# Optimization experiments

Hardware: AMD Instinct MI355X
Metric: run time of the kernel (lower is better)

Reference implementation:

```python
import jax, jax.numpy as jnp
import numpy as np

B, T, C, H = 2, 2048, 1024, 16
N = C // H
TM_DIM, TD_DIM = 32, 64
EPS = 1e-5 * 8 ** 2  # GroupNorm eps from the module


def setup_inputs() -> dict:
    key = jax.random.key(0)
    ks = jax.random.split(key, 16)
    nrm = lambda k, shp, s: jax.random.normal(k, shp, dtype=jnp.float32) * s
    uni = lambda k, shp, a: jax.random.uniform(k, shp, jnp.float32, -a, a)
    ddd = (jnp.arange(C, dtype=jnp.float32) / C).reshape(1, 1, C)
    return {
        "x": nrm(ks[0], (B, T, C), 1.0),
        "time_maa_x": 1.0 - ddd ** 0.5,
        "time_maa_w": 1.0 - ddd ** 0.5,
        "time_maa_k": 1.0 - ddd ** 0.5,
        "time_maa_v": 1.0 - (ddd ** 0.5 + 0.15),
        "time_maa_r": 1.0 - ddd ** 0.25,
        "time_maa_g": 1.0 - ddd ** 0.25,
        "time_maa_w1": uni(ks[1], (C, 5 * TM_DIM), 1e-4),
        "time_maa_w2": uni(ks[2], (5, TM_DIM, C), 1e-4),
        "time_decay": jnp.linspace(-6.0, -1.0, C).astype(jnp.float32).reshape(1, 1, C),
        "time_decay_w1": uni(ks[3], (C, TD_DIM), 1e-4),
        "time_decay_w2": uni(ks[4], (TD_DIM, C), 1e-4),
        "time_faaaa": nrm(ks[5], (H, N), 0.1),
        "W_r": nrm(ks[6], (C, C), C ** -0.5),
        "W_k": nrm(ks[7], (C, C), C ** -0.5),
        "W_v": nrm(ks[8], (C, C), C ** -0.5),
        "W_g": nrm(ks[9], (C, C), C ** -0.5),
        "W_o": nrm(ks[10], (C, C), C ** -0.5),
        "ln_w": jnp.ones((C,), jnp.float32),
        "ln_b": jnp.zeros((C,), jnp.float32),
    }


def _forward(x, tmx, tmw, tmk, tmv, tmr, tmg, maa_w1, maa_w2, tdecay, td_w1,
             td_w2, u, Wr, Wk, Wv, Wg, Wo, ln_w, ln_b):
    Bq, Tq, Cq = x.shape
    # time_shift: x[t-1] with zero at t=0
    xx = jnp.concatenate([jnp.zeros_like(x[:, :1]), x[:, :-1]], axis=1) - x
    xxx = x + xx * tmx
    t5 = jnp.tanh(xxx @ maa_w1).reshape(Bq, Tq, 5, TM_DIM)
    m = jnp.einsum('btfe,fec->fbtc', t5, maa_w2)  # [5,B,T,C] data-dependent mix
    xw = x + xx * (tmw + m[0])
    xk = x + xx * (tmk + m[1])
    xv = x + xx * (tmv + m[2])
    xr = x + xx * (tmr + m[3])
    xg = x + xx * (tmg + m[4])
    r = xr @ Wr
    k = xk @ Wk
    v = xv @ Wv
    g = jax.nn.silu(xg @ Wg)
    w = tdecay + jnp.tanh(xw @ td_w1) @ td_w2          # [B,T,C] log-log decay
    decay = jnp.exp(-jnp.exp(w))                        # in (0,1)
    to_tbhn = lambda a: a.reshape(Bq, Tq, H, N).transpose(1, 0, 2, 3)
    rT, kT, vT, dT = (to_tbhn(a) for a in (r, k, v, decay))

    def step(S, inp):  # S: [B,H,N,N] (key_dim i, value_dim j)
        r_t, k_t, v_t, d_t = inp
        kv = k_t[..., :, None] * v_t[..., None, :]
        y = jnp.einsum('bhi,bhij->bhj', r_t, S + u[None, :, :, None] * kv)
        return d_t[..., None] * S + kv, y

    S0 = jnp.zeros((Bq, H, N, N), x.dtype)
    _, ys = jax.lax.scan(step, S0, (rT, kT, vT, dT))
    y = ys.transpose(1, 0, 2, 3).reshape(Bq, Tq, Cq)
    # GroupNorm with H groups over channels
    yh = y.reshape(Bq, Tq, H, N)
    mu = yh.mean(-1, keepdims=True)
    var = yh.var(-1, keepdims=True)
    yn = (yh - mu) / jnp.sqrt(var + EPS)
    yn = (yn * ln_w.reshape(H, N) + ln_b.reshape(H, N)).reshape(Bq, Tq, Cq)
    return (yn * g) @ Wo


def reference(x, time_maa_x, time_maa_w, time_maa_k, time_maa_v, time_maa_r,
              time_maa_g, time_maa_w1, time_maa_w2, time_decay, time_decay_w1,
              time_decay_w2, time_faaaa, W_r, W_k, W_v, W_g, W_o, ln_w, ln_b):
    return _forward(x, time_maa_x, time_maa_w, time_maa_k, time_maa_v,
                    time_maa_r, time_maa_g, time_maa_w1, time_maa_w2,
                    time_decay, time_decay_w1, time_decay_w2, time_faaaa,
                    W_r, W_k, W_v, W_g, W_o, ln_w, ln_b)
```

## Files before the change

kernel.cpp:

```cpp
#include <hip/hip_runtime.h>
#include <hip/hip_bf16.h>
#include <cstdint>
#include <cstddef>

#define B_ 2
#define T_ 2048
#define C_ 1024
#define H_ 16
#define NCH 32
#define CHL 64

typedef unsigned short ushort_t;
typedef __bf16 bf16x8 __attribute__((ext_vector_type(8)));
typedef float f32x4 __attribute__((ext_vector_type(4)));

__device__ __forceinline__ ushort_t f2bf(float f) {
  union { float f; uint32_t u; } x; x.f = f;
  uint32_t r = x.u + 0x7fffu + ((x.u >> 16) & 1u);
  return (ushort_t)(r >> 16);
}
__device__ __forceinline__ float bf2f(ushort_t h) {
  union { uint32_t u; float f; } x; x.u = (uint32_t)h << 16; return x.f;
}

__device__ __forceinline__ void gload16(const void* g, void* l) {
  __builtin_amdgcn_global_load_lds(
      (const __attribute__((address_space(1))) void*)g,
      (__attribute__((address_space(3))) void*)l, 16, 0, 0);
}

#define FENCE() asm volatile("" ::: "memory")
#define BAR() do { FENCE(); __builtin_amdgcn_s_barrier(); FENCE(); } while (0)

__device__ __forceinline__ void stb(ushort_t* tile, int row, int col, ushort_t v) {
  *(ushort_t*)((char*)tile + row * 128 + ((col * 2) ^ ((row & 7) << 4))) = v;
}
__device__ __forceinline__ bf16x8 ldb(const ushort_t* tile, int row, int kbyte) {
  return *(const bf16x8*)((const char*)tile + row * 128 + (kbyte ^ ((row & 7) << 4)));
}

struct TDesc { const float* src; ushort_t* dst; int R, Cc, Cpad; };
struct TArgs { TDesc d[9]; };

__global__ __launch_bounds__(256) void transpose_cvt(TArgs args) {
  TDesc D = args.d[blockIdx.z];
  int c0 = blockIdx.x * 32, r0 = blockIdx.y * 32;
  if (c0 >= D.Cpad || r0 >= D.R) return;
  __shared__ float tile[32][33];
  int tx = threadIdx.x & 31, ty = threadIdx.x >> 5;
#pragma unroll
  for (int i = 0; i < 32; i += 8) {
    int r = r0 + ty + i, c = c0 + tx;
    tile[ty + i][tx] = (r < D.R && c < D.Cc) ? D.src[(size_t)r * D.Cc + c] : 0.f;
  }
  __syncthreads();
#pragma unroll
  for (int i = 0; i < 32; i += 8) {
    int c = c0 + ty + i, r = r0 + tx;
    if (c < D.Cpad && r < D.R) D.dst[(size_t)c * D.R + r] = f2bf(tile[tx][ty + i]);
  }
}

__global__ __launch_bounds__(256) void prep_kernel(
    const float* __restrict__ x, const float* __restrict__ tmx,
    float* __restrict__ xx, ushort_t* __restrict__ xxx) {
  size_t idx = ((size_t)blockIdx.x * 256 + threadIdx.x) * 4;
  int tt = (int)((idx >> 10) & (T_ - 1));
  int c = (int)(idx & (C_ - 1));
  float4 xv = *(const float4*)&x[idx];
  float4 xp;
  if (tt == 0) { xp.x = xp.y = xp.z = xp.w = 0.f; }
  else xp = *(const float4*)&x[idx - C_];
  float4 tm = *(const float4*)&tmx[c];
  float4 d;
  d.x = xp.x - xv.x; d.y = xp.y - xv.y; d.z = xp.z - xv.z; d.w = xp.w - xv.w;
  *(float4*)&xx[idx] = d;
  xxx[idx + 0] = f2bf(xv.x + d.x * tm.x);
  xxx[idx + 1] = f2bf(xv.y + d.y * tm.y);
  xxx[idx + 2] = f2bf(xv.z + d.z * tm.z);
  xxx[idx + 3] = f2bf(xv.w + d.w * tm.w);
}

template <int EPI>
__global__ __launch_bounds__(256) void gemm_bt(
    const ushort_t* __restrict__ A, int lda,
    const ushort_t* __restrict__ Bt, int ldb,
    void* __restrict__ Cp, int ldc, int K,
    const float* __restrict__ aux2) {
  __shared__ ushort_t sA[128 * 32];
  __shared__ ushort_t sB[128 * 32];
  const int t = threadIdx.x;
  const int l = t & 63;
  const int w = t >> 6;
  const int wm = w >> 1, wn = w & 1;
  const int m0 = blockIdx.x * 128, n0 = blockIdx.y * 128;
  const int lr = l & 15;
  const int lk = (l >> 4) * 8;

  f32x4 acc[4][4] = {};

  for (int kt = 0; kt < K; kt += 32) {
    __syncthreads();
#pragma unroll
    for (int it = 0; it < 2; ++it) {
      int cbase = it * 256 + w * 64;
      int ca = cbase + l;
      int row = ca >> 2, kc = ca & 3;
      gload16(A + (size_t)(m0 + row) * lda + kt + kc * 8, (char*)sA + (size_t)cbase * 16);
      gload16(Bt + (size_t)(n0 + row) * ldb + kt + kc * 8, (char*)sB + (size_t)cbase * 16);
    }
    __syncthreads();
    bf16x8 af[4], bfr[4];
#pragma unroll
    for (int mi = 0; mi < 4; ++mi)
      af[mi] = *(const bf16x8*)&sA[(wm * 64 + mi * 16 + lr) * 32 + lk];
#pragma unroll
    for (int ni = 0; ni < 4; ++ni)
      bfr[ni] = *(const bf16x8*)&sB[(wn * 64 + ni * 16 + lr) * 32 + lk];
#pragma unroll
    for (int mi = 0; mi < 4; ++mi)
#pragma unroll
      for (int ni = 0; ni < 4; ++ni)
        acc[mi][ni] = __builtin_amdgcn_mfma_f32_16x16x32_bf16(af[mi], bfr[ni], acc[mi][ni], 0, 0, 0);
  }
#pragma unroll
  for (int mi = 0; mi < 4; ++mi) {
#pragma unroll
    for (int ni = 0; ni < 4; ++ni) {
      int col = n0 + wn * 64 + ni * 16 + lr;
#pragma unroll
      for (int r = 0; r < 4; ++r) {
        int row = m0 + wm * 64 + mi * 16 + (l >> 4) * 4 + r;
        float v = acc[mi][ni][r];
        size_t idx = (size_t)row * ldc + col;
        if constexpr (EPI == 0) {
          ((float*)Cp)[idx] = v;
        } else if constexpr (EPI == 4) {
          ((float*)Cp)[idx] = __expf(aux2[col] + v);
        }
      }
    }
  }
}

__global__ __launch_bounds__(256) void gemm_bt64(
    const ushort_t* __restrict__ A, int lda,
    const ushort_t* __restrict__ Bt, int ldb,
    ushort_t* __restrict__ Cp, int ldc, int K) {
  __shared__ ushort_t sA[64 * 32];
  __shared__ ushort_t sB[128 * 32];
  const int t = threadIdx.x;
  const int l = t & 63;
  const int w = t >> 6;
  const int m0 = blockIdx.x * 64, n0 = blockIdx.y * 128;
  const int lr = l & 15, lk = (l >> 4) * 8;

  f32x4 acc[4][2] = {};
  for (int kt = 0; kt < K; kt += 32) {
    __syncthreads();
    {
      int row = t >> 2, kc = t & 3;
      gload16(A + (size_t)(m0 + row) * lda + kt + kc * 8, (char*)sA + w * 1024);
    }
#pragma unroll
    for (int it = 0; it < 2; ++it) {
      int ca = it * 256 + t;
      int row = ca >> 2, kc = ca & 3;
      gload16(Bt + (size_t)(n0 + row) * ldb + kt + kc * 8,
              (char*)sB + it * 4096 + w * 1024);
    }
    __syncthreads();
    bf16x8 af[4], bfr[2];
#pragma unroll
    for (int mi = 0; mi < 4; ++mi)
      af[mi] = *(const bf16x8*)&sA[(mi * 16 + lr) * 32 + lk];
#pragma unroll
    for (int ni = 0; ni < 2; ++ni)
      bfr[ni] = *(const bf16x8*)&sB[(w * 32 + ni * 16 + lr) * 32 + lk];
#pragma unroll
    for (int mi = 0; mi < 4; ++mi)
#pragma unroll
      for (int ni = 0; ni < 2; ++ni)
        acc[mi][ni] = __builtin_amdgcn_mfma_f32_16x16x32_bf16(af[mi], bfr[ni], acc[mi][ni], 0, 0, 0);
  }
#pragma unroll
  for (int mi = 0; mi < 4; ++mi)
#pragma unroll
    for (int ni = 0; ni < 2; ++ni) {
      int col = n0 + w * 32 + ni * 16 + lr;
#pragma unroll
      for (int r = 0; r < 4; ++r) {
        int row = m0 + mi * 16 + (l >> 4) * 4 + r;
        Cp[(size_t)row * ldc + col] = f2bf(tanhf(acc[mi][ni][r]));
      }
    }
}

struct PDesc { const ushort_t* A; const ushort_t* Bt; float* C; int epi; };
struct PArgs { PDesc d[4]; };

__device__ __forceinline__ bf16x8 ldsw(const ushort_t* t_, int row, int slot) {
  return *(const bf16x8*)((const char*)t_ + row * 128 + (((slot ^ (row & 7)) << 4)));
}

__global__ __launch_bounds__(512, 2) void gemm_proj256(PArgs args) {
  PDesc D = args.d[blockIdx.z];
  __shared__ ushort_t sA0[256 * 64], sB0[256 * 64], sA1[256 * 64], sB1[256 * 64];
  const int tid = threadIdx.x;
  const int w = tid >> 6, l = tid & 63;
  const int wm = w >> 2, wn = w & 3;
  const int lr = l & 15, hi4 = l >> 4;
  const int m0 = blockIdx.x * 256, n0 = blockIdx.y * 256;

  const int srow = tid >> 3;
  const int scol = ((tid & 7) ^ (srow & 7)) << 3;
  const ushort_t* Ag = D.A + (size_t)(m0 + srow) * C_ + scol;
  const ushort_t* Bg = D.Bt + (size_t)(n0 + srow) * C_ + scol;
  const int wb = w * 1024;

  f32x4 acc[8][4] = {};

#define STAGE256(sa, sb, kt)                                        \
  do {                                                              \
    const ushort_t* ap_ = Ag + (kt);                                \
    const ushort_t* bp_ = Bg + (kt);                                \
    gload16(ap_,            (char*)(sa) + 0 * 8192 + wb);           \
    gload16(ap_ +  64 * C_, (char*)(sa) + 1 * 8192 + wb);           \
    gload16(ap_ + 128 * C_, (char*)(sa) + 2 * 8192 + wb);           \
    gload16(ap_ + 192 * C_, (char*)(sa) + 3 * 8192 + wb);           \
    gload16(bp_,            (char*)(sb) + 0 * 8192 + wb);           \
    gload16(bp_ +  64 * C_, (char*)(sb) + 1 * 8192 + wb);           \
    gload16(bp_ + 128 * C_, (char*)(sb) + 2 * 8192 + wb);           \
    gload16(bp_ + 192 * C_, (char*)(sb) + 3 * 8192 + wb);           \
  } while (0)

#define KSTEP256(CA, CB, t)                                                  \
  do {                                                                       \
    if ((t) < 15) asm volatile("s_waitcnt vmcnt(8)" ::: "memory");           \
    else          asm volatile("s_waitcnt vmcnt(0)" ::: "memory");           \
    BAR();                                                                   \
    _Pragma("unroll")                                                        \
    for (int kk = 0; kk < 2; ++kk) {                                         \
      bf16x8 bfrag[4];                                                       \
      _Pragma("unroll")                                                      \
      for (int ni = 0; ni < 4; ++ni)                                         \
        bfrag[ni] = ldsw(CB, wn * 64 + ni * 16 + lr, kk * 4 + hi4);          \
      __builtin_amdgcn_s_setprio(1);                                         \
      _Pragma("unroll")                                                      \
      for (int mi = 0; mi < 8; ++mi) {                                       \
        bf16x8 af = ldsw(CA, wm * 128 + mi * 16 + lr, kk * 4 + hi4);         \
        _Pragma("unroll")                                                    \
        for (int ni = 0; ni < 4; ++ni)                                       \
          acc[mi][ni] = __builtin_amdgcn_mfma_f32_16x16x32_bf16(             \
              af, bfrag[ni], acc[mi][ni], 0, 0, 0);                          \
      }                                                                      \
      __builtin_amdgcn_s_setprio(0);                                         \
    }                                                                        \
    asm volatile("s_waitcnt lgkmcnt(0)" ::: "memory");                       \
    __builtin_amdgcn_sched_barrier(0);                                       \
    BAR();                                                                   \
    if ((t) < 14) STAGE256(CA, CB, ((t) + 2) * 64);                          \
  } while (0)

  STAGE256(sA0, sB0, 0);
  STAGE256(sA1, sB1, 64);

#pragma unroll 1
  for (int tt = 0; tt < 8; ++tt) {
    KSTEP256(sA0, sB0, tt * 2);
    KSTEP256(sA1, sB1, tt * 2 + 1);
  }

  const int epi = D.epi;
#pragma unroll
  for (int mi = 0; mi < 8; ++mi)
#pragma unroll
    for (int ni = 0; ni < 4; ++ni) {
      int col = n0 + wn * 64 + ni * 16 + lr;
#pragma unroll
      for (int r = 0; r < 4; ++r) {
        int row = m0 + wm * 128 + mi * 16 + hi4 * 4 + r;
        float v = acc[mi][ni][r];
        if (epi) v = v / (1.f + __expf(-v));
        D.C[(size_t)row * C_ + col] = v;
      }
    }
#undef KSTEP256
#undef STAGE256
}

struct MixArgs { const float* tm[5]; ushort_t* dst[5]; };

__global__ __launch_bounds__(256) void fused_mix(
    const float* __restrict__ x, const float* __restrict__ xx,
    const ushort_t* __restrict__ t5, const ushort_t* __restrict__ w2t,
    MixArgs margs) {
  __shared__ float xs[64 * 128];
  __shared__ float xxs[64 * 128];
  __shared__ ushort_t sA[64 * 32];
  __shared__ ushort_t sB[128 * 32];
  const int t = threadIdx.x;
  const int l = t & 63;
  const int w = t >> 6;
  const int wm = w >> 1, wn = w & 1;
  const int m0 = blockIdx.x * 64, n0 = blockIdx.y * 128;
  const int lr = l & 15;
  const int lk = (l >> 4) * 8;

#pragma unroll
  for (int it = 0; it < 8; ++it) {
    int row = it * 8 + (t >> 5);
    int c16 = t & 31;
    gload16(x + (size_t)(m0 + row) * C_ + n0 + c16 * 4, (char*)xs + row * 512 + c16 * 16);
    gload16(xx + (size_t)(m0 + row) * C_ + n0 + c16 * 4, (char*)xxs + row * 512 + c16 * 16);
  }

  for (int f = 0; f < 5; ++f) {
    __syncthreads();
    {
      int row = t >> 2, c8 = t & 3;
      gload16(t5 + (size_t)(m0 + row) * 256 + f * 32 + c8 * 8, (char*)sA + t * 16);
    }
#pragma unroll
    for (int it = 0; it < 2; ++it) {
      int row = it * 64 + (t >> 2), c8 = t & 3;
      gload16(w2t + (size_t)(n0 + row) * 160 + f * 32 + c8 * 8,
              (char*)sB + it * 4096 + t * 16);
    }
    __syncthreads();
    bf16x8 af[2], bfr[4];
#pragma unroll
    for (int mi = 0; mi < 2; ++mi)
      af[mi] = *(const bf16x8*)&sA[(wm * 32 + mi * 16 + lr) * 32 + lk];
#pragma unroll
    for (int ni = 0; ni < 4; ++ni)
      bfr[ni] = *(const bf16x8*)&sB[(wn * 64 + ni * 16 + lr) * 32 + lk];
    f32x4 acc[2][4] = {};
#pragma unroll
    for (int mi = 0; mi < 2; ++mi)
#pragma unroll
      for (int ni = 0; ni < 4; ++ni)
        acc[mi][ni] = __builtin_amdgcn_mfma_f32_16x16x32_bf16(af[mi], bfr[ni], acc[mi][ni], 0, 0, 0);
    const float* tmf = margs.tm[f];
    ushort_t* dst = margs.dst[f];
#pragma unroll
    for (int mi = 0; mi < 2; ++mi) {
#pragma unroll
      for (int ni = 0; ni < 4; ++ni) {
        int cl = wn * 64 + ni * 16 + lr;
        int col = n0 + cl;
        float tmv = tmf[col];
#pragma unroll
        for (int r = 0; r < 4; ++r) {
          int rl = wm * 32 + mi * 16 + (l >> 4) * 4 + r;
          int row = m0 + rl;
          float xv = xs[rl * 128 + cl];
          float xxv = xxs[rl * 128 + cl];
          dst[(size_t)row * C_ + col] = f2bf(xv + xxv * (tmv + acc[mi][ni][r]));
        }
      }
    }
  }
}

__global__ __launch_bounds__(256) void chunk_local(
    const float* __restrict__ rx, const float* __restrict__ kx,
    const float* __restrict__ vx, const float* __restrict__ lamx,
    const float* __restrict__ u, float* __restrict__ Mt,
    float* __restrict__ aLg, ushort_t* __restrict__ rAg,
    float* __restrict__ yo) {
  int c = blockIdx.x, bh = blockIdx.y;
  int b = bh >> 4, h = bh & 15;
  __shared__ ushort_t sRA[64 * 64], sKA[64 * 64], sKh[64 * 64], sKl[64 * 64],
                      sVh[64 * 64], sVl[64 * 64], sP[64 * 64];
  __shared__ float qsum[4][64];
  __shared__ float ruk[64];
  const int tid = threadIdx.x;
  const int i = tid & 63;
  const int q = tid >> 6;
  size_t base = ((size_t)b * T_ + (size_t)c * CHL) * C_ + h * 64;
  size_t cb = ((size_t)c * 32 + bh);

  float lam[16];
  float run = 0.f;
#pragma unroll
  for (int s = 0; s < 16; ++s) {
    lam[s] = lamx[base + (size_t)(q * 16 + s) * C_ + i];
    run += lam[s];
  }
  qsum[q][i] = run;
  __syncthreads();
  float pre = 0.f, ct = 0.f;
#pragma unroll
  for (int qq = 0; qq < 4; ++qq) {
    float vq = qsum[qq][i];
    ct += vq;
    if (qq < q) pre += vq;
  }
  float uu = u[h * 64 + i];
  float ci = pre;
#pragma unroll
  for (int s = 0; s < 16; ++s) {
    int t = q * 16 + s;
    ci += lam[s];
    float cl = ci - lam[s];
    size_t o = base + (size_t)t * C_ + i;
    float rv = rx[o], kv = kx[o], vv = vx[o];
    ushort_t ra = f2bf(rv * __expf(-cl));
    stb(sRA, t, i, ra);
    rAg[cb * 4096 + t * 64 + i] = ra;
    stb(sKA, t, i, f2bf(kv * __expf(ci)));
    float kal = kv * __expf(ci - ct);
    ushort_t khv = f2bf(kal);
    stb(sKh, i, t, khv);
    stb(sKl, i, t, f2bf(kal - bf2f(khv)));
    ushort_t vhv = f2bf(vv);
    stb(sVh, i, t, vhv);
    stb(sVl, i, t, f2bf(vv - bf2f(vhv)));
    float rr = rv * uu * kv;
#pragma unroll
    for (int m = 32; m; m >>= 1) rr += __shfl_xor(rr, m);
    if (i == 0) ruk[t] = rr;
  }
  if (q == 0) aLg[cb * 64 + i] = __expf(-ct);
  __syncthreads();

  const int l = tid & 63, w = tid >> 6;
  const int wm = w >> 1, wn = w & 1;
  const int lr = l & 15, hi4 = l >> 4;

  {
    f32x4 accP[2][2] = {};
#pragma unroll
    for (int kk = 0; kk < 2; ++kk) {
      bf16x8 af[2], bf_[2];
#pragma unroll
      for (int mi = 0; mi < 2; ++mi) af[mi] = ldb(sRA, wm * 32 + mi * 16 + lr, kk * 64 + hi4 * 16);
#pragma unroll
      for (int ni = 0; ni < 2; ++ni) bf_[ni] = ldb(sKA, wn * 32 + ni * 16 + lr, kk * 64 + hi4 * 16);
#pragma unroll
      for (int mi = 0; mi < 2; ++mi)
#pragma unroll
        for (int ni = 0; ni < 2; ++ni)
          accP[mi][ni] = __builtin_amdgcn_mfma_f32_16x16x32_bf16(af[mi], bf_[ni], accP[mi][ni], 0, 0, 0);
    }
#pragma unroll
    for (int mi = 0; mi < 2; ++mi)
#pragma unroll
      for (int ni = 0; ni < 2; ++ni)
#pragma unroll
        for (int r = 0; r < 4; ++r) {
          int tl = wm * 32 + mi * 16 + hi4 * 4 + r, sl = wn * 32 + ni * 16 + lr;
          float v = accP[mi][ni][r];
          v = sl < tl ? v : (sl == tl ? ruk[tl] : 0.f);
          stb(sP, tl, sl, f2bf(v));
        }
  }
  __syncthreads();

  f32x4 accY[2][2] = {}, accM[2][2] = {};
#pragma unroll
  for (int kk = 0; kk < 2; ++kk) {
    bf16x8 pa[2], vhA[2], vlA[2], vhB[2], vlB[2], khB[2], klB[2];
#pragma unroll
    for (int mi = 0; mi < 2; ++mi) {
      int rw = wm * 32 + mi * 16 + lr;
      pa[mi] = ldb(sP, rw, kk * 64 + hi4 * 16);
      vhA[mi] = ldb(sVh, rw, kk * 64 + hi4 * 16);
      vlA[mi] = ldb(sVl, rw, kk * 64 + hi4 * 16);
    }
#pragma unroll
    for (int ni = 0; ni < 2; ++ni) {
      int rw = wn * 32 + ni * 16 + lr;
      vhB[ni] = ldb(sVh, rw, kk * 64 + hi4 * 16);
      vlB[ni] = ldb(sVl, rw, kk * 64 + hi4 * 16);
      khB[ni] = ldb(sKh, rw, kk * 64 + hi4 * 16);
      klB[ni] = ldb(sKl, rw, kk * 64 + hi4 * 16);
    }
#pragma unroll
    for (int mi = 0; mi < 2; ++mi)
#pragma unroll
      for (int ni = 0; ni < 2; ++ni) {
        accY[mi][ni] = __builtin_amdgcn_mfma_f32_16x16x32_bf16(pa[mi], vhB[ni], accY[mi][ni], 0, 0, 0);
        accY[mi][ni] = __builtin_amdgcn_mfma_f32_16x16x32_bf16(pa[mi], vlB[ni], accY[mi][ni], 0, 0, 0);
        accM[mi][ni] = __builtin_amdgcn_mfma_f32_16x16x32_bf16(vhA[mi], khB[ni], accM[mi][ni], 0, 0, 0);
        accM[mi][ni] = __builtin_amdgcn_mfma_f32_16x16x32_bf16(vhA[mi], klB[ni], accM[mi][ni], 0, 0, 0);
        accM[mi][ni] = __builtin_amdgcn_mfma_f32_16x16x32_bf16(vlA[mi], khB[ni], accM[mi][ni], 0, 0, 0);
      }
  }
#pragma unroll
  for (int mi = 0; mi < 2; ++mi)
#pragma unroll
    for (int ni = 0; ni < 2; ++ni)
#pragma unroll
      for (int r = 0; r < 4; ++r) {
        int rw = wm * 32 + mi * 16 + hi4 * 4 + r;
        int cw = wn * 32 + ni * 16 + lr;
        yo[base + (size_t)rw * C_ + cw] = accY[mi][ni][r];
        Mt[cb * 4096 + rw * 64 + cw] = accM[mi][ni][r];
      }
}

__global__ __launch_bounds__(256) void combine2(
    const float* __restrict__ Mt, const float* __restrict__ aLg,
    ushort_t* __restrict__ S0h, ushort_t* __restrict__ S0l) {
  int bh = blockIdx.x >> 2;
  int ij = ((blockIdx.x & 3) * 256 + threadIdx.x) * 4;
  int i = ij & 63;
  float4 s = {0.f, 0.f, 0.f, 0.f};
  for (int c = 0; c < NCH; ++c) {
    size_t o = ((size_t)c * 32 + bh) * 4096 + ij;
    float4 m = *(const float4*)&Mt[o];
    float4 p = *(const float4*)&aLg[((size_t)c * 32 + bh) * 64 + i];
    ushort4 hi, lo;
    hi.x = f2bf(s.x); lo.x = f2bf(s.x - bf2f(hi.x));
    hi.y = f2bf(s.y); lo.y = f2bf(s.y - bf2f(hi.y));
    hi.z = f2bf(s.z); lo.z = f2bf(s.z - bf2f(hi.z));
    hi.w = f2bf(s.w); lo.w = f2bf(s.w - bf2f(hi.w));
    *(ushort4*)&S0h[o] = hi;
    *(ushort4*)&S0l[o] = lo;
    s.x = p.x * s.x + m.x; s.y = p.y * s.y + m.y;
    s.z = p.z * s.z + m.z; s.w = p.w * s.w + m.w;
  }
}

__global__ __launch_bounds__(256) void inter_gn(
    const ushort_t* __restrict__ rAg, const ushort_t* __restrict__ S0h,
    const ushort_t* __restrict__ S0l, const float* __restrict__ yin,
    const float* __restrict__ gx, const float* __restrict__ lnw,
    const float* __restrict__ lnb, ushort_t* __restrict__ Z) {
  int c = blockIdx.x, bh = blockIdx.y;
  int b = bh >> 4, h = bh & 15;
  __shared__ ushort_t sRA[64 * 64], sSh[64 * 64], sSl[64 * 64];
  __shared__ float st[64][2][2];
  const int tid = threadIdx.x;
  size_t cb = ((size_t)c * 32 + bh) * 4096;
#pragma unroll
  for (int it = 0; it < 2; ++it) {
    int lb = tid * 32 + it * 16;
    int row = lb >> 7, wi = lb & 127;
    int so = row * 128 + (wi ^ ((row & 7) << 4));
    *(uint4*)((char*)sRA + so) = *(const uint4*)((const char*)(rAg + cb) + lb);
    *(uint4*)((char*)sSh + so) = *(const uint4*)((const char*)(S0h + cb) + lb);
    *(uint4*)((char*)sSl + so) = *(const uint4*)((const char*)(S0l + cb) + lb);
  }
  const int l = tid & 63, w = tid >> 6;
  const int wm = w >> 1, wn = w & 1;
  const int lr = l & 15, hi4 = l >> 4;
  size_t base = ((size_t)b * T_ + (size_t)c * CHL) * C_ + h * 64;

  f32x4 acc[2][2];
#pragma unroll
  for (int mi = 0; mi < 2; ++mi)
#pragma unroll
    for (int ni = 0; ni < 2; ++ni)
#pragma unroll
      for (int r = 0; r < 4; ++r)
        acc[mi][ni][r] = yin[base + (size_t)(wm * 32 + mi * 16 + hi4 * 4 + r) * C_ +
                             wn * 32 + ni * 16 + lr];
  __syncthreads();
#pragma unroll
  for (int kk = 0; kk < 2; ++kk) {
    bf16x8 af[2], bh_[2], bl_[2];
#pragma unroll
    for (int mi = 0; mi < 2; ++mi) af[mi] = ldb(sRA, wm * 32 + mi * 16 + lr, kk * 64 + hi4 * 16);
#pragma unroll
    for (int ni = 0; ni < 2; ++ni) {
      bh_[ni] = ldb(sSh, wn * 32 + ni * 16 + lr, kk * 64 + hi4 * 16);
      bl_[ni] = ldb(sSl, wn * 32 + ni * 16 + lr, kk * 64 + hi4 * 16);
    }
#pragma unroll
    for (int mi = 0; mi < 2; ++mi)
#pragma unroll
      for (int ni = 0; ni < 2; ++ni) {
        acc[mi][ni] = __builtin_amdgcn_mfma_f32_16x16x32_bf16(af[mi], bh_[ni], acc[mi][ni], 0, 0, 0);
        acc[mi][ni] = __builtin_amdgcn_mfma_f32_16x16x32_bf16(af[mi], bl_[ni], acc[mi][ni], 0, 0, 0);
      }
  }
#pragma unroll
  for (int mi = 0; mi < 2; ++mi)
#pragma unroll
    for (int r = 0; r < 4; ++r) {
      int row = wm * 32 + mi * 16 + hi4 * 4 + r;
      float s1 = acc[mi][0][r] + acc[mi][1][r];
      float s2 = acc[mi][0][r] * acc[mi][0][r] + acc[mi][1][r] * acc[mi][1][r];
#pragma unroll
      for (int m = 1; m < 16; m <<= 1) { s1 += __shfl_xor(s1, m); s2 += __shfl_xor(s2, m); }
      if (lr == 0) { st[row][wn][0] = s1; st[row][wn][1] = s2; }
    }
  __syncthreads();
#pragma unroll
  for (int mi = 0; mi < 2; ++mi)
#pragma unroll
    for (int ni = 0; ni < 2; ++ni)
#pragma unroll
      for (int r = 0; r < 4; ++r) {
        int row = wm * 32 + mi * 16 + hi4 * 4 + r;
        int jl = wn * 32 + ni * 16 + lr;
        float S1 = st[row][0][0] + st[row][1][0];
        float S2 = st[row][0][1] + st[row][1][1];
        float mu = S1 * (1.f / 64.f);
        float var = S2 * (1.f / 64.f) - mu * mu;
        float rs = rsqrtf(var + 6.4e-4f);
        int col = h * 64 + jl;
        size_t o = base + (size_t)row * C_ + jl;
        float yn = (acc[mi][ni][r] - mu) * rs * lnw[col] + lnb[col];
        Z[o] = f2bf(yn * gx[o]);
      }
}

extern "C" void kernel_launch(void* const* d_in, const int* in_sizes, int n_in,
                              void* d_out, int out_size, void* d_ws, size_t ws_size,
                              hipStream_t stream) {
  const float* x    = (const float*)d_in[0];
  const float* tmx  = (const float*)d_in[1];
  const float* tmw  = (const float*)d_in[2];
  const float* tmk  = (const float*)d_in[3];
  const float* tmv  = (const float*)d_in[4];
  const float* tmr  = (const float*)d_in[5];
  const float* tmg  = (const float*)d_in[6];
  const float* maaw1 = (const float*)d_in[7];
  const float* maaw2 = (const float*)d_in[8];
  const float* tdec = (const float*)d_in[9];
  const float* tdw1 = (const float*)d_in[10];
  const float* tdw2 = (const float*)d_in[11];
  const float* u    = (const float*)d_in[12];
  const float* Wr   = (const float*)d_in[13];
  const float* Wk   = (const float*)d_in[14];
  const float* Wv   = (const float*)d_in[15];
  const float* Wg   = (const float*)d_in[16];
  const float* Wo   = (const float*)d_in[17];
  const float* lnw  = (const float*)d_in[18];
  const float* lnb  = (const float*)d_in[19];

  char* ws = (char*)d_ws;
  const size_t MB = 1ull << 20;
  float*    xx     = (float*)(ws + 0);
  ushort_t* xxx    = (ushort_t*)(ws + 16 * MB);
  ushort_t* WrT    = (ushort_t*)(ws + 24 * MB);
  ushort_t* WkT    = (ushort_t*)(ws + 26 * MB);
  ushort_t* WvT    = (ushort_t*)(ws + 28 * MB);
  ushort_t* WgT    = (ushort_t*)(ws + 30 * MB);
  ushort_t* WoT    = (ushort_t*)(ws + 32 * MB);
  ushort_t* maaW1T = (ushort_t*)(ws + 34 * MB);
  ushort_t* tdW1T  = (ushort_t*)(ws + 35 * MB);
  ushort_t* tdW2T  = (ushort_t*)(ws + 35 * MB + 256 * 1024);
  ushort_t* maaW2T = (ushort_t*)(ws + 35 * MB + 512 * 1024);
  ushort_t* t5     = (ushort_t*)(ws + 36 * MB);
  ushort_t* t5d    = (ushort_t*)(ws + 38 * MB);
  ushort_t* Xm[5];
  for (int f = 0; f < 5; ++f) Xm[f] = (ushort_t*)(ws + 40 * MB + (size_t)f * 8 * MB);
  float*    Mtb = (float*)(ws + 40 * MB);
  ushort_t* S0h = (ushort_t*)(ws + 56 * MB);
  ushort_t* S0l = (ushort_t*)(ws + 64 * MB);
  ushort_t* rAg = (ushort_t*)(ws + 72 * MB);
  float* rb   = (float*)(ws + 80 * MB);
  float* kb   = (float*)(ws + 96 * MB);
  float* vb   = (float*)(ws + 112 * MB);
  float* gb   = (float*)(ws + 128 * MB);
  float* lam  = (float*)(ws + 144 * MB);
  float* aLg  = (float*)(ws + 160 * MB);
  float* yb   = (float*)(ws + 0);
  ushort_t* Zb = (ushort_t*)(ws + 16 * MB);

  TArgs ta;
  ta.d[0] = TDesc{Wr,    WrT,    1024, 1024, 1024};
  ta.d[1] = TDesc{Wk,    WkT,    1024, 1024, 1024};
  ta.d[2] = TDesc{Wv,    WvT,    1024, 1024, 1024};
  ta.d[3] = TDesc{Wg,    WgT,    1024, 1024, 1024};
  ta.d[4] = TDesc{Wo,    WoT,    1024, 1024, 1024};
  ta.d[5] = TDesc{maaw1, maaW1T, 1024, 160,  256};
  ta.d[6] = TDesc{tdw1,  tdW1T,  1024, 64,   128};
  ta.d[7] = TDesc{tdw2,  tdW2T,  64,   1024, 1024};
  ta.d[8] = TDesc{maaw2, maaW2T, 160,  1024, 1024};
  transpose_cvt<<<dim3(32, 32, 9), 256, 0, stream>>>(ta);

  prep_kernel<<<(B_ * T_ * C_) / 1024, 256, 0, stream>>>(x, tmx, xx, xxx);

  gemm_bt64<<<dim3(64, 2), 256, 0, stream>>>(xxx, C_, maaW1T, C_, t5, 256, C_);

  MixArgs ma;
  ma.tm[0] = tmw; ma.tm[1] = tmk; ma.tm[2] = tmv; ma.tm[3] = tmr; ma.tm[4] = tmg;
  for (int f = 0; f < 5; ++f) ma.dst[f] = Xm[f];
  fused_mix<<<dim3(64, 8), 256, 0, stream>>>(x, xx, t5, maaW2T, ma);

  PArgs pa;
  pa.d[0] = PDesc{Xm[3], WrT, rb, 0};
  pa.d[1] = PDesc{Xm[1], WkT, kb, 0};
  pa.d[2] = PDesc{Xm[2], WvT, vb, 0};
  pa.d[3] = PDesc{Xm[4], WgT, gb, 1};
  gemm_proj256<<<dim3(16, 4, 4), 512, 0, stream>>>(pa);

  gemm_bt64<<<dim3(64, 1), 256, 0, stream>>>(Xm[0], C_, tdW1T, C_, t5d, 128, C_);
  gemm_bt<4><<<dim3(32, 8), 256, 0, stream>>>(t5d, 128, tdW2T, 64, lam, C_, 64, tdec);

  chunk_local<<<dim3(NCH, B_ * H_), 256, 0, stream>>>(rb, kb, vb, lam, u, Mtb, aLg, rAg, yb);
  combine2<<<128, 256, 0, stream>>>(Mtb, aLg, S0h, S0l);
  inter_gn<<<dim3(NCH, B_ * H_), 256, 0, stream>>>(rAg, S0h, S0l, yb, gb, lnw, lnb, Zb);

  gemm_bt<0><<<dim3(32, 8), 256, 0, stream>>>(Zb, C_, WoT, C_, (float*)d_out, C_, C_, nullptr);
}
```

Before: 210.9 us.

## Restructure projection GEMM into fine-grained interleaved load/MFMA pipeline

Rewrites the 256x256 projection GEMM main loop so that global-to-LDS loads for the next k-tile are issued in four pieces, each interleaved with a quarter of the current tile's MFMA work and separated by barriers. The LDS layout changes to 32-column half-k slabs with a 4-way XOR swizzle, and launch bounds drop from 2 to 1 block per CU. The aim is to hide global load latency behind MFMA issue in a ping-pong schedule like hipBLASLt's. In exchange it adds many more barriers per k-tile and lowers occupancy, which could expose latency if the interleaving does not line up.

Measured after the change: 216.4 us. 2.6% more time.

```diff
diff --git a/kernel.cpp b/kernel.cpp
--- a/kernel.cpp
+++ b/kernel.cpp
@@ -199,76 +199,118 @@
 struct PDesc { const ushort_t* A; const ushort_t* Bt; float* C; int epi; };
 struct PArgs { PDesc d[4]; };
 
-__device__ __forceinline__ bf16x8 ldsw(const ushort_t* t_, int row, int slot) {
-  return *(const bf16x8*)((const char*)t_ + row * 128 + (((slot ^ (row & 7)) << 4)));
-}
-
-__global__ __launch_bounds__(512, 2) void gemm_proj256(PArgs args) {
+__global__ __launch_bounds__(512, 1) void gemm_proj256(PArgs args) {
   PDesc D = args.d[blockIdx.z];
-  __shared__ ushort_t sA0[256 * 64], sB0[256 * 64], sA1[256 * 64], sB1[256 * 64];
+  __shared__ ushort_t sA0[16384], sA1[16384];
+  __shared__ ushort_t sB0[16384], sB1[16384];
   const int tid = threadIdx.x;
   const int w = tid >> 6, l = tid & 63;
   const int wm = w >> 2, wn = w & 3;
   const int lr = l & 15, hi4 = l >> 4;
   const int m0 = blockIdx.x * 256, n0 = blockIdx.y * 256;
 
-  const int srow = tid >> 3;
-  const int scol = ((tid & 7) ^ (srow & 7)) << 3;
-  const ushort_t* Ag = D.A + (size_t)(m0 + srow) * C_ + scol;
-  const ushort_t* Bg = D.Bt + (size_t)(n0 + srow) * C_ + scol;
-  const int wb = w * 1024;
+  const int tid16 = tid * 16;
+  const int srow = tid >> 2;
+  const int acol8 = ((tid & 3) ^ (srow & 3)) << 3;
+  const ushort_t* Ag0 = D.A + (size_t)(m0 + srow) * C_ + acol8;
+  const ushort_t* Ag1 = D.A + (size_t)(m0 + 128 + srow) * C_ + acol8;
+  const ushort_t* Bg0 = D.Bt + (size_t)(n0 + srow) * C_ + acol8;
+  const ushort_t* Bg1 = D.Bt + (size_t)(n0 + 128 + srow) * C_ + acol8;
 
   f32x4 acc[8][4] = {};
 
-#define STAGE256(sa, sb, kt)                                        \
-  do {                                                              \
-    const ushort_t* ap_ = Ag + (kt);                                \
-    const ushort_t* bp_ = Bg + (kt);                                \
-    gload16(ap_,            (char*)(sa) + 0 * 8192 + wb);           \
-    gload16(ap_ +  64 * C_, (char*)(sa) + 1 * 8192 + wb);           \
-    gload16(ap_ + 128 * C_, (char*)(sa) + 2 * 8192 + wb);           \
-    gload16(ap_ + 192 * C_, (char*)(sa) + 3 * 8192 + wb);           \
-    gload16(bp_,            (char*)(sb) + 0 * 8192 + wb);           \
-    gload16(bp_ +  64 * C_, (char*)(sb) + 1 * 8192 + wb);           \
-    gload16(bp_ + 128 * C_, (char*)(sb) + 2 * 8192 + wb);           \
-    gload16(bp_ + 192 * C_, (char*)(sb) + 3 * 8192 + wb);           \
+#define LDA256(CA, kk, mh, ms)                                                \
+  (*(const bf16x8*)((const char*)(CA) + ((kk)*2 + wm) * 8192 +                \
+                    ((mh)*64 + (ms)*16 + lr) * 64 + ((hi4 ^ (lr & 3)) << 4)))
+#define LDB256(CB, kk, ni)                                                    \
+  (*(const bf16x8*)((const char*)(CB) + (kk)*16384 +                          \
+                    (wn * 64 + (ni)*16 + lr) * 64 + ((hi4 ^ (lr & 3)) << 4)))
+
+#define MFMA16(arow)                                                          \
+  do {                                                                        \
+    __builtin_amdgcn_s_setprio(1);                                            \
+    _Pragma("unroll")                                                         \
+    for (int ms = 0; ms < 4; ++ms) {                                          \
+      _Pragma("unroll")                                                       \
+      for (int ni = 0; ni < 4; ++ni)                                          \
+        acc[(arow) + ms][ni] = __builtin_amdgcn_mfma_f32_16x16x32_bf16(       \
+            afr[ms], bfr[ni], acc[(arow) + ms][ni], 0, 0, 0);                 \
+    }                                                                         \
+    __builtin_amdgcn_s_setprio(0);                                            \
   } while (0)
 
-#define KSTEP256(CA, CB, t)                                                  \
-  do {                                                                       \
-    if ((t) < 15) asm volatile("s_waitcnt vmcnt(8)" ::: "memory");           \
-    else          asm volatile("s_waitcnt vmcnt(0)" ::: "memory");           \
-    BAR();                                                                   \
-    _Pragma("unroll")                                                        \
-    for (int kk = 0; kk < 2; ++kk) {                                         \
-      bf16x8 bfrag[4];                                                       \
-      _Pragma("unroll")                                                      \
-      for (int ni = 0; ni < 4; ++ni)                                         \
-        bfrag[ni] = ldsw(CB, wn * 64 + ni * 16 + lr, kk * 4 + hi4);          \
-      __builtin_amdgcn_s_setprio(1);                                         \
-      _Pragma("unroll")                                                      \
-      for (int mi = 0; mi < 8; ++mi) {                                       \
-        bf16x8 af = ldsw(CA, wm * 128 + mi * 16 + lr, kk * 4 + hi4);         \
-        _Pragma("unroll")                                                    \
-        for (int ni = 0; ni < 4; ++ni)                                       \
-          acc[mi][ni] = __builtin_amdgcn_mfma_f32_16x16x32_bf16(             \
-              af, bfrag[ni], acc[mi][ni], 0, 0, 0);                          \
-      }                                                                      \
-      __builtin_amdgcn_s_setprio(0);                                         \
-    }                                                                        \
-    asm volatile("s_waitcnt lgkmcnt(0)" ::: "memory");                       \
-    __builtin_amdgcn_sched_barrier(0);                                       \
-    BAR();                                                                   \
-    if ((t) < 14) STAGE256(CA, CB, ((t) + 2) * 64);                          \
+#define LGKM0()                                                               \
+  do {                                                                        \
+    asm volatile("s_waitcnt lgkmcnt(0)" ::: "memory");                        \
+    __builtin_amdgcn_sched_barrier(0);                                        \
   } while (0)
 
-  STAGE256(sA0, sB0, 0);
-  STAGE256(sA1, sB1, 64);
+#define TILE256(CA, CB, NA, NB, J, KN)                                        \
+  do {                                                                        \
+    const bool st_ = (J) < 15;                                                \
+    bf16x8 afr[4], bfr[4];                                                    \
+                                                       \
+    _Pragma("unroll") for (int ni = 0; ni < 4; ++ni) bfr[ni] = LDB256(CB, 0, ni); \
+    _Pragma("unroll") for (int ms = 0; ms < 4; ++ms) afr[ms] = LDA256(CA, 0, 0, ms); \
+    if (st_) {                                                                \
+      gload16(Ag0 + (KN), (char*)(NA) + 0 * 8192 + tid16);                    \
+      gload16(Ag1 + (KN), (char*)(NA) + 1 * 8192 + tid16);                    \
+    }                                                                         \
+    BAR();                                                                    \
+    LGKM0();                                                                  \
+    MFMA16(0);                                                                \
+    BAR();                                                                    \
+                                                       \
+    _Pragma("unroll") for (int ms = 0; ms < 4; ++ms) afr[ms] = LDA256(CA, 0, 1, ms); \
+    if (st_) {                                                                \
+      gload16(Bg0 + (KN), (char*)(NB) + 0 * 8192 + tid16);                    \
+      gload16(Bg1 + (KN), (char*)(NB) + 1 * 8192 + tid16);                    \
+    }                                                                         \
+    BAR();                                                                    \
+    LGKM0();                                                                  \
+    MFMA16(4);                                                                \
+    if (st_) asm volatile("s_waitcnt vmcnt(4)" ::: "memory");                 \
+    else     asm volatile("s_waitcnt vmcnt(0)" ::: "memory");                 \
+    BAR();                                                                    \
+                                                       \
+    _Pragma("unroll") for (int ni = 0; ni < 4; ++ni) bfr[ni] = LDB256(CB, 1, ni); \
+    _Pragma("unroll") for (int ms = 0; ms < 4; ++ms) afr[ms] = LDA256(CA, 1, 0, ms); \
+    if (st_) {                                                                \
+      gload16(Ag0 + (KN) + 32, (char*)(NA) + 2 * 8192 + tid16);               \
+      gload16(Ag1 + (KN) + 32, (char*)(NA) + 3 * 8192 + tid16);               \
+    }                                                                         \
+    BAR();                                                                    \
+    LGKM0();                                                                  \
+    MFMA16(0);                                                                \
+    BAR();                                                                    \
+                                                       \
+    _Pragma("unroll") for (int ms = 0; ms < 4; ++ms) afr[ms] = LDA256(CA, 1, 1, ms); \
+    if (st_) {                                                                \
+      gload16(Bg0 + (KN) + 32, (char*)(NB) + 2 * 8192 + tid16);               \
+      gload16(Bg1 + (KN) + 32, (char*)(NB) + 3 * 8192 + tid16);               \
+    }                                                                         \
+    BAR();                                                                    \
+    LGKM0();                                                                  \
+    MFMA16(4);                                                                \
+    if (st_) asm volatile("s_waitcnt vmcnt(4)" ::: "memory");                 \
+    BAR();                                                                    \
+  } while (0)
+
+  gload16(Ag0, (char*)sA0 + 0 * 8192 + tid16);
+  gload16(Ag1, (char*)sA0 + 1 * 8192 + tid16);
+  gload16(Bg0, (char*)sB0 + 0 * 8192 + tid16);
+  gload16(Bg1, (char*)sB0 + 1 * 8192 + tid16);
+  gload16(Ag0 + 32, (char*)sA0 + 2 * 8192 + tid16);
+  gload16(Ag1 + 32, (char*)sA0 + 3 * 8192 + tid16);
+  gload16(Bg0 + 32, (char*)sB0 + 2 * 8192 + tid16);
+  gload16(Bg1 + 32, (char*)sB0 + 3 * 8192 + tid16);
+  asm volatile("s_waitcnt vmcnt(4)" ::: "memory");
+  BAR();
 
 #pragma unroll 1
-  for (int tt = 0; tt < 8; ++tt) {
-    KSTEP256(sA0, sB0, tt * 2);
-    KSTEP256(sA1, sB1, tt * 2 + 1);
+  for (int j = 0; j < 16; j += 2) {
+    TILE256(sA0, sB0, sA1, sB1, j, (j + 1) * 64);
+    TILE256(sA1, sB1, sA0, sB0, j + 1, (j + 2) * 64);
   }
 
   const int epi = D.epi;
@@ -285,8 +327,11 @@
         D.C[(size_t)row * C_ + col] = v;
       }
     }
-#undef KSTEP256
-#undef STAGE256
+#undef TILE256
+#undef LGKM0
+#undef MFMA16
+#undef LDB256
+#undef LDA256
 }
 
 struct MixArgs { const float* tm[5]; ushort_t* dst[5]; };
```
